# Kernel optimization log

Measured on AMD Instinct MI355X. Metric: run time of the kernel, lower is better.

Reference implementation:

```python
import jax, jax.numpy as jnp
import numpy as np

NUM_TABLES = 26
ROWS = 100000
EMB = 64
B = 4096
L = 32  # num_lookups per bag
BOT = [256, 512, 256, 64]
TOP = [EMB * (1 + NUM_TABLES), 512, 256, 1]


def _mlp_params(key, dims):
    params = []
    for i in range(len(dims) - 1):
        din, dout = dims[i], dims[i + 1]
        kw, kb, key = jax.random.split(key, 3)
        sw = np.sqrt(2.0 / (din + dout)).astype(np.float32)
        sb = np.sqrt(1.0 / dout).astype(np.float32)
        params.append((jax.random.normal(kw, (dout, din), jnp.float32) * sw,
                       jax.random.normal(kb, (dout,), jnp.float32) * sb))
    return params


def setup_inputs() -> dict:
    key = jax.random.key(0)
    k0, k1, k2, k3, k4 = jax.random.split(key, 5)
    inp = {}
    inp["x_dense"] = jax.random.normal(k0, (B, BOT[0]), jnp.float32)
    inp["x_indices"] = jax.random.randint(k1, (NUM_TABLES, B, L), 0, ROWS)
    bound = np.sqrt(1.0 / ROWS).astype(np.float32)
    inp["emb_tables"] = jax.random.uniform(k2, (NUM_TABLES, ROWS, EMB), jnp.float32, -bound, bound)
    for i, (w, b) in enumerate(_mlp_params(k3, BOT)):
        inp[f"bot_w{i}"] = w
        inp[f"bot_b{i}"] = b
    for i, (w, b) in enumerate(_mlp_params(k4, TOP)):
        inp[f"top_w{i}"] = w
        inp[f"top_b{i}"] = b
    return inp


def _forward(x_dense, x_indices, emb_tables, bot, top):
    # bottom MLP: Linear+ReLU per layer
    h = x_dense
    for w, b in bot:
        h = jax.nn.relu(h @ w.T + b)
    # multi-table EmbeddingBag(mode='sum'): gather rows then sum over bag dim
    # pooled: [T, B, E]
    pooled = jax.vmap(lambda tbl, idx: jnp.take(tbl, idx, axis=0).sum(axis=1))(emb_tables, x_indices)
    emb = jnp.transpose(pooled, (1, 0, 2)).reshape(x_dense.shape[0], -1)  # [B, T*E]
    z = jnp.concatenate([h, emb], axis=1)  # [B, E*(1+T)]
    # top MLP: ReLU on all but last, sigmoid on last
    n = len(top)
    for i, (w, b) in enumerate(top):
        z = z @ w.T + b
        z = jax.nn.sigmoid(z) if i == n - 1 else jax.nn.relu(z)
    return z


def reference(x_dense, x_indices, emb_tables,
              bot_w0, bot_b0, bot_w1, bot_b1, bot_w2, bot_b2,
              top_w0, top_b0, top_w1, top_b1, top_w2, top_b2):
    bot = [(bot_w0, bot_b0), (bot_w1, bot_b1), (bot_w2, bot_b2)]
    top = [(top_w0, top_b0), (top_w1, top_b1), (top_w2, top_b2)]
    return _forward(x_dense, x_indices, emb_tables, bot, top)
```

## Files before the change

### kernel.cpp

```cpp
#include <hip/hip_runtime.h>
#include <hip/hip_bf16.h>
#include <math.h>

typedef __attribute__((ext_vector_type(8))) short short8;
typedef __attribute__((ext_vector_type(4))) float f32x4;

#define NUM_TABLES 26
#define ROWS 100000
#define EMB 64
#define BATCH 4096
#define LOOKUPS 32
#define ZDIM 1728
#define CAST_BLOCKS 512
#define EMBED_BLOCKS (NUM_TABLES * BATCH / 4)

__device__ __forceinline__ unsigned short f2bf(float f) {
  unsigned int u = __float_as_uint(f);
  u += 0x7FFFu + ((u >> 16) & 1u);
  return (unsigned short)(u >> 16);
}
__device__ __forceinline__ float bf2f(unsigned short h) {
  return __uint_as_float(((unsigned int)h) << 16);
}

__device__ __forceinline__ void gload16(const void* g, void* l) {
  __builtin_amdgcn_global_load_lds(
      (const __attribute__((address_space(1))) void*)g,
      (__attribute__((address_space(3))) void*)l, 16, 0, 0);
}

struct CastArgs {
  const float* s[6];
  unsigned short* d[6];
  int n4[6];
  int total;
};

__global__ void embed_cast(CastArgs a, const int* __restrict__ idx,
                           const float* __restrict__ tables,
                           unsigned short* __restrict__ z) {
  if (blockIdx.x < CAST_BLOCKS) {
    for (int i = blockIdx.x * blockDim.x + threadIdx.x; i < a.total;
         i += CAST_BLOCKS * blockDim.x) {
      int r = i;
      #pragma unroll
      for (int sg = 0; sg < 6; ++sg) {
        if (r < a.n4[sg]) {
          float4 v = ((const float4*)a.s[sg])[r];
          ushort4 o;
          o.x = f2bf(v.x); o.y = f2bf(v.y); o.z = f2bf(v.z); o.w = f2bf(v.w);
          ((ushort4*)a.d[sg])[r] = o;
          break;
        }
        r -= a.n4[sg];
      }
    }
    return;
  }
  int g = (int)(((blockIdx.x - CAST_BLOCKS) << 2) + (threadIdx.x >> 6));
  int lane = threadIdx.x & 63;
  int t = g >> 12;
  int b = g & 4095;
  const int* ip = idx + ((size_t)t * BATCH + b) * LOOKUPS;
  int myidx = (lane < LOOKUPS) ? ip[lane] : 0;
  const float* tbl = tables + (size_t)t * ROWS * EMB;
  int grp = lane >> 4;
  int e4 = lane & 15;
  float4 acc = {0.f, 0.f, 0.f, 0.f};
  #pragma unroll
  for (int it = 0; it < 8; ++it) {
    int r = __shfl(myidx, it * 4 + grp, 64);
    float4 v = ((const float4*)(tbl + (size_t)r * EMB))[e4];
    acc.x += v.x; acc.y += v.y; acc.z += v.z; acc.w += v.w;
  }
  #pragma unroll
  for (int m = 16; m <= 32; m <<= 1) {
    acc.x += __shfl_xor(acc.x, m, 64);
    acc.y += __shfl_xor(acc.y, m, 64);
    acc.z += __shfl_xor(acc.z, m, 64);
    acc.w += __shfl_xor(acc.w, m, 64);
  }
  if (lane < 16) {
    ushort4 o;
    o.x = f2bf(acc.x); o.y = f2bf(acc.y); o.z = f2bf(acc.z); o.w = f2bf(acc.w);
    *(ushort4*)&z[(size_t)b * ZDIM + EMB + t * EMB + e4 * 4] = o;
  }
}

template<int ACT>
__global__ __launch_bounds__(256) void gemm64s(
    const unsigned short* __restrict__ A,
    const unsigned short* __restrict__ W,
    const float* __restrict__ bias,
    unsigned short* __restrict__ C,
    int M, int N, int K, int ldc) {
  __shared__ unsigned short lds[2][64][64];

  int t = threadIdx.x;
  int lane = t & 63;
  int wid = t >> 6;
  int wr = wid >> 1;
  int wc = wid & 1;

  int ntn = N >> 6;
  int tm = blockIdx.x / ntn;
  int tn = blockIdx.x - tm * ntn;

  int srow = lane >> 3;
  int schunk = (lane & 7) ^ (srow & 7);
  const unsigned short* Ap0 = A + (size_t)(tm * 64 + wid * 16 + srow) * K + schunk * 8;
  const unsigned short* Wp0 = W + (size_t)(tn * 64 + wid * 16 + srow) * K + schunk * 8;
  size_t rowK8 = (size_t)8 * K;

  f32x4 acc[2][2];
  #pragma unroll
  for (int m = 0; m < 2; ++m)
    #pragma unroll
    for (int n = 0; n < 2; ++n)
      acc[m][n] = (f32x4){0.f, 0.f, 0.f, 0.f};

  int ra = wr * 32 + (lane & 15);
  int rb = wc * 32 + (lane & 15);
  int cidx = lane >> 4;
  int sA = ra & 7, sB = rb & 7;

  for (int k0 = 0; k0 < K; k0 += 64) {
    #pragma unroll
    for (int j = 0; j < 2; ++j) {
      gload16(Ap0 + (size_t)k0 + j * rowK8, &lds[0][wid * 16 + j * 8][0]);
      gload16(Wp0 + (size_t)k0 + j * rowK8, &lds[1][wid * 16 + j * 8][0]);
    }
    __syncthreads();

    const char* bA = (const char*)&lds[0][0][0];
    const char* bB = (const char*)&lds[1][0][0];
    #pragma unroll
    for (int kc = 0; kc < 2; ++kc) {
      int c = kc * 4 + cidx;
      short8 a0 = *(const short8*)(bA + ra * 128 + ((c ^ sA) << 4));
      short8 a1 = *(const short8*)(bA + (ra + 16) * 128 + ((c ^ sA) << 4));
      short8 b0 = *(const short8*)(bB + rb * 128 + ((c ^ sB) << 4));
      short8 b1 = *(const short8*)(bB + (rb + 16) * 128 + ((c ^ sB) << 4));
      acc[0][0] = __builtin_amdgcn_mfma_f32_16x16x32_bf16(a0, b0, acc[0][0], 0, 0, 0);
      acc[0][1] = __builtin_amdgcn_mfma_f32_16x16x32_bf16(a0, b1, acc[0][1], 0, 0, 0);
      acc[1][0] = __builtin_amdgcn_mfma_f32_16x16x32_bf16(a1, b0, acc[1][0], 0, 0, 0);
      acc[1][1] = __builtin_amdgcn_mfma_f32_16x16x32_bf16(a1, b1, acc[1][1], 0, 0, 0);
    }
    __syncthreads();
  }

  #pragma unroll
  for (int m = 0; m < 2; ++m) {
    int drow = tm * 64 + wr * 32 + m * 16 + ((lane >> 4) << 2);
    #pragma unroll
    for (int n = 0; n < 2; ++n) {
      int dcol = tn * 64 + wc * 32 + n * 16 + (lane & 15);
      float bv = bias[dcol];
      #pragma unroll
      for (int r = 0; r < 4; ++r) {
        float v = acc[m][n][r] + bv;
        if (ACT == 1) v = v > 0.f ? v : 0.f;
        C[(size_t)(drow + r) * ldc + dcol] = f2bf(v);
      }
    }
  }
}

template<int ACT>
__global__ void gemm16(const unsigned short* __restrict__ A,
                       const unsigned short* __restrict__ W,
                       const float* __restrict__ bias,
                       unsigned short* __restrict__ C,
                       int M, int N, int K, int ldc) {
  int lane = threadIdx.x & 63;
  int gw = (int)((blockIdx.x * blockDim.x + threadIdx.x) >> 6);
  int ntn = N >> 4;
  int tm = gw / ntn;
  int tn = gw - tm * ntn;
  if (tm >= (M >> 4)) return;

  int arow = (tm << 4) + (lane & 15);
  int wrow = (tn << 4) + (lane & 15);
  int kb = (lane >> 4) << 3;

  const short8* Ap = (const short8*)(A + (size_t)arow * K + kb);
  const short8* Wp = (const short8*)(W + (size_t)wrow * K + kb);

  f32x4 acc = {0.f, 0.f, 0.f, 0.f};
  int steps = K >> 5;
  #pragma unroll 8
  for (int s = 0; s < steps; ++s) {
    short8 a = Ap[s * 4];
    short8 b = Wp[s * 4];
    acc = __builtin_amdgcn_mfma_f32_16x16x32_bf16(a, b, acc, 0, 0, 0);
  }

  int dcol = (tn << 4) + (lane & 15);
  int drow = (tm << 4) + ((lane >> 4) << 2);
  float bv = bias[dcol];
  #pragma unroll
  for (int r = 0; r < 4; ++r) {
    float v = acc[r] + bv;
    if (ACT == 1) v = v > 0.f ? v : 0.f;
    C[(size_t)(drow + r) * ldc + dcol] = f2bf(v);
  }
}

__global__ void final_layer(const unsigned short* __restrict__ z2,
                            const float* __restrict__ w,
                            const float* __restrict__ bias,
                            float* __restrict__ out) {
  int g = (int)((blockIdx.x * blockDim.x + threadIdx.x) >> 6);
  int lane = threadIdx.x & 63;
  const unsigned short* zp = z2 + (size_t)g * 256;
  float s = 0.f;
  #pragma unroll
  for (int k = 0; k < 256; k += 64)
    s += bf2f(zp[k + lane]) * w[k + lane];
  #pragma unroll
  for (int off = 32; off > 0; off >>= 1)
    s += __shfl_down(s, off, 64);
  if (lane == 0) out[g] = 1.f / (1.f + expf(-(s + bias[0])));
}

extern "C" void kernel_launch(void* const* d_in, const int* in_sizes, int n_in,
                              void* d_out, int out_size, void* d_ws, size_t ws_size,
                              hipStream_t stream) {
  const float* x_dense = (const float*)d_in[0];
  const int*   x_idx   = (const int*)d_in[1];
  const float* tables  = (const float*)d_in[2];
  const float* bw0 = (const float*)d_in[3];  const float* bb0 = (const float*)d_in[4];
  const float* bw1 = (const float*)d_in[5];  const float* bb1 = (const float*)d_in[6];
  const float* bw2 = (const float*)d_in[7];  const float* bb2 = (const float*)d_in[8];
  const float* tw0 = (const float*)d_in[9];  const float* tb0 = (const float*)d_in[10];
  const float* tw1 = (const float*)d_in[11]; const float* tb1 = (const float*)d_in[12];
  const float* tw2 = (const float*)d_in[13]; const float* tb2 = (const float*)d_in[14];
  float* out = (float*)d_out;

  char* ws = (char*)d_ws;
  size_t off = 0;
  auto alloc = [&](size_t bytes) { void* p = ws + off; off += (bytes + 255) & ~(size_t)255; return p; };
  unsigned short* xdb  = (unsigned short*)alloc((size_t)BATCH * 256 * 2);
  unsigned short* bw0b = (unsigned short*)alloc((size_t)512 * 256 * 2);
  unsigned short* bw1b = (unsigned short*)alloc((size_t)256 * 512 * 2);
  unsigned short* bw2b = (unsigned short*)alloc((size_t)64 * 256 * 2);
  unsigned short* tw0b = (unsigned short*)alloc((size_t)512 * ZDIM * 2);
  unsigned short* tw1b = (unsigned short*)alloc((size_t)256 * 512 * 2);
  unsigned short* h0   = (unsigned short*)alloc((size_t)BATCH * 512 * 2);
  unsigned short* h1   = (unsigned short*)alloc((size_t)BATCH * 256 * 2);
  unsigned short* z    = (unsigned short*)alloc((size_t)BATCH * ZDIM * 2);
  unsigned short* z1   = (unsigned short*)alloc((size_t)BATCH * 512 * 2);
  unsigned short* z2   = (unsigned short*)alloc((size_t)BATCH * 256 * 2);

  {
    CastArgs a;
    a.s[0] = x_dense; a.d[0] = xdb;  a.n4[0] = BATCH * 256 / 4;
    a.s[1] = bw0;     a.d[1] = bw0b; a.n4[1] = 512 * 256 / 4;
    a.s[2] = bw1;     a.d[2] = bw1b; a.n4[2] = 256 * 512 / 4;
    a.s[3] = bw2;     a.d[3] = bw2b; a.n4[3] = 64 * 256 / 4;
    a.s[4] = tw0;     a.d[4] = tw0b; a.n4[4] = 512 * ZDIM / 4;
    a.s[5] = tw1;     a.d[5] = tw1b; a.n4[5] = 256 * 512 / 4;
    a.total = a.n4[0] + a.n4[1] + a.n4[2] + a.n4[3] + a.n4[4] + a.n4[5];
    embed_cast<<<CAST_BLOCKS + EMBED_BLOCKS, 256, 0, stream>>>(a, x_idx, tables, z);
  }

  auto gemm = [&](const unsigned short* A, const unsigned short* W, const float* bias,
                  unsigned short* C, int M, int N, int K, int ldc, int relu) {
    if (N >= 128) {
      int blocks = (M >> 6) * (N >> 6);
      if (relu)
        gemm64s<1><<<blocks, 256, 0, stream>>>(A, W, bias, C, M, N, K, ldc);
      else
        gemm64s<0><<<blocks, 256, 0, stream>>>(A, W, bias, C, M, N, K, ldc);
    } else {
      int tiles = (M >> 4) * (N >> 4);
      if (relu)
        gemm16<1><<<tiles / 4, 256, 0, stream>>>(A, W, bias, C, M, N, K, ldc);
      else
        gemm16<0><<<tiles / 4, 256, 0, stream>>>(A, W, bias, C, M, N, K, ldc);
    }
  };

  gemm(xdb, bw0b, bb0, h0, BATCH, 512, 256, 512, 1);
  gemm(h0,  bw1b, bb1, h1, BATCH, 256, 512, 256, 1);
  gemm(h1,  bw2b, bb2, z,  BATCH, 64, 256, ZDIM, 1);

  gemm(z,  tw0b, tb0, z1, BATCH, 512, ZDIM, 512, 1);
  gemm(z1, tw1b, tb1, z2, BATCH, 256, 512, 256, 1);

  final_layer<<<BATCH / 4, 256, 0, stream>>>(z2, tw2, tb2, out);
}
```

Measured before the change: 182.2 us.

## Fuse bottom MLP into embedding kernel with per-block LDS-resident activations

Moves the three bottom-MLP layers into the same launch as the embedding-bag gather. Each of the new blocks handles 16 batch rows, keeps intermediate activations in swizzled LDS, and converts fp32 weights to bf16 on the fly instead of using a separate cast pass. This removes three GEMM launches, the cast of the bottom weights and input, and the global round trips for h0/h1, and lets the bottom MLP overlap with the memory-bound gather. The cost is that every block re-reads the full bottom weight matrices from global/L2 and converts them redundantly. The bottom-MLP blocks may also underuse MFMA because each handles only 16 rows.

Result: faster. 177.1 us (-2.8%).

```diff
diff --git a/kernel.cpp b/kernel.cpp
--- a/kernel.cpp
+++ b/kernel.cpp
@@ -11,7 +11,9 @@
 #define BATCH 4096
 #define LOOKUPS 32
 #define ZDIM 1728
-#define CAST_BLOCKS 512
+
+#define CAST_BLOCKS 128
+#define BOT_BLOCKS 256
 #define EMBED_BLOCKS (NUM_TABLES * BATCH / 4)
 
 __device__ __forceinline__ unsigned short f2bf(float f) {
@@ -29,41 +31,163 @@
       (__attribute__((address_space(3))) void*)l, 16, 0, 0);
 }
 
-struct CastArgs {
-  const float* s[6];
-  unsigned short* d[6];
-  int n4[6];
-  int total;
+__device__ __forceinline__ short8 wfrag_f32(const float* __restrict__ W, int K,
+                                            int colbase, int l, int kc) {
+  const float* p = W + (size_t)(colbase + (l & 15)) * K + kc * 32 + ((l >> 4) << 3);
+  float4 u = *(const float4*)p;
+  float4 v = *(const float4*)(p + 4);
+  short8 f;
+  f[0] = (short)f2bf(u.x); f[1] = (short)f2bf(u.y);
+  f[2] = (short)f2bf(u.z); f[3] = (short)f2bf(u.w);
+  f[4] = (short)f2bf(v.x); f[5] = (short)f2bf(v.y);
+  f[6] = (short)f2bf(v.z); f[7] = (short)f2bf(v.w);
+  return f;
+}
+
+struct MegaArgs {
+  const float* cast_s[2];
+  unsigned short* cast_d[2];
+  int cast_n4[2];
+  int cast_total;
+  const float* x_dense;
+  const float* bw0; const float* bb0;
+  const float* bw1; const float* bb1;
+  const float* bw2; const float* bb2;
+  const int* idx;
+  const float* tables;
+  unsigned short* z;
 };
 
-__global__ void embed_cast(CastArgs a, const int* __restrict__ idx,
-                           const float* __restrict__ tables,
-                           unsigned short* __restrict__ z) {
+__global__ void mega(MegaArgs a) {
+  __shared__ unsigned short xb[16][256];
+  __shared__ unsigned short h0[16][512];
+
   if (blockIdx.x < CAST_BLOCKS) {
-    for (int i = blockIdx.x * blockDim.x + threadIdx.x; i < a.total;
+    for (int i = blockIdx.x * blockDim.x + threadIdx.x; i < a.cast_total;
          i += CAST_BLOCKS * blockDim.x) {
       int r = i;
       #pragma unroll
-      for (int sg = 0; sg < 6; ++sg) {
-        if (r < a.n4[sg]) {
-          float4 v = ((const float4*)a.s[sg])[r];
+      for (int sg = 0; sg < 2; ++sg) {
+        if (r < a.cast_n4[sg]) {
+          float4 v = ((const float4*)a.cast_s[sg])[r];
           ushort4 o;
           o.x = f2bf(v.x); o.y = f2bf(v.y); o.z = f2bf(v.z); o.w = f2bf(v.w);
-          ((ushort4*)a.d[sg])[r] = o;
+          ((ushort4*)a.cast_d[sg])[r] = o;
           break;
         }
-        r -= a.n4[sg];
+        r -= a.cast_n4[sg];
       }
     }
     return;
   }
-  int g = (int)(((blockIdx.x - CAST_BLOCKS) << 2) + (threadIdx.x >> 6));
+
+  if (blockIdx.x < CAST_BLOCKS + BOT_BLOCKS) {
+    int b0 = (int)(blockIdx.x - CAST_BLOCKS) << 4;
+    int w = threadIdx.x >> 6;
+    int l = threadIdx.x & 63;
+
+    #pragma unroll
+    for (int i = 0; i < 4; ++i) {
+      int flat = i * 256 + threadIdx.x;
+      int row = flat >> 6;
+      int c4 = flat & 63;
+      float4 v = *(const float4*)(a.x_dense + (size_t)(b0 + row) * 256 + c4 * 4);
+      int chunk = c4 >> 1;
+      int scol = ((chunk ^ (row & 7)) << 3) | ((c4 & 1) << 2);
+      ushort4 o;
+      o.x = f2bf(v.x); o.y = f2bf(v.y); o.z = f2bf(v.z); o.w = f2bf(v.w);
+      *(ushort4*)&xb[row][scol] = o;
+    }
+    __syncthreads();
+
+    int arow = l & 15;
+    int sA = arow & 7;
+    const char* xbp = (const char*)&xb[0][0];
+    const char* h0p = (const char*)&h0[0][0];
+
+    f32x4 acc0[8];
+    #pragma unroll
+    for (int n = 0; n < 8; ++n) acc0[n] = (f32x4){0.f, 0.f, 0.f, 0.f};
+    for (int kc = 0; kc < 8; ++kc) {
+      int c = kc * 4 + (l >> 4);
+      short8 av = *(const short8*)(xbp + arow * 512 + ((c ^ sA) << 4));
+      #pragma unroll
+      for (int n = 0; n < 8; ++n) {
+        short8 bv = wfrag_f32(a.bw0, 256, w * 128 + n * 16, l, kc);
+        acc0[n] = __builtin_amdgcn_mfma_f32_16x16x32_bf16(av, bv, acc0[n], 0, 0, 0);
+      }
+    }
+    #pragma unroll
+    for (int n = 0; n < 8; ++n) {
+      int col = w * 128 + n * 16 + (l & 15);
+      float bv = a.bb0[col];
+      int chunk = col >> 3;
+      #pragma unroll
+      for (int r = 0; r < 4; ++r) {
+        int row = ((l >> 4) << 2) + r;
+        float val = acc0[n][r] + bv;
+        val = val > 0.f ? val : 0.f;
+        h0[row][((chunk ^ (row & 7)) << 3) | (col & 7)] = f2bf(val);
+      }
+    }
+    __syncthreads();
+
+    f32x4 acc1[4];
+    #pragma unroll
+    for (int n = 0; n < 4; ++n) acc1[n] = (f32x4){0.f, 0.f, 0.f, 0.f};
+    for (int kc = 0; kc < 16; ++kc) {
+      int c = kc * 4 + (l >> 4);
+      short8 av = *(const short8*)(h0p + arow * 1024 + ((c ^ sA) << 4));
+      #pragma unroll
+      for (int n = 0; n < 4; ++n) {
+        short8 bv = wfrag_f32(a.bw1, 512, w * 64 + n * 16, l, kc);
+        acc1[n] = __builtin_amdgcn_mfma_f32_16x16x32_bf16(av, bv, acc1[n], 0, 0, 0);
+      }
+    }
+    __syncthreads();
+    #pragma unroll
+    for (int n = 0; n < 4; ++n) {
+      int col = w * 64 + n * 16 + (l & 15);
+      float bv = a.bb1[col];
+      int chunk = col >> 3;
+      #pragma unroll
+      for (int r = 0; r < 4; ++r) {
+        int row = ((l >> 4) << 2) + r;
+        float val = acc1[n][r] + bv;
+        val = val > 0.f ? val : 0.f;
+        xb[row][((chunk ^ (row & 7)) << 3) | (col & 7)] = f2bf(val);
+      }
+    }
+    __syncthreads();
+
+    f32x4 acc2 = (f32x4){0.f, 0.f, 0.f, 0.f};
+    for (int kc = 0; kc < 8; ++kc) {
+      int c = kc * 4 + (l >> 4);
+      short8 av = *(const short8*)(xbp + arow * 512 + ((c ^ sA) << 4));
+      short8 bv = wfrag_f32(a.bw2, 256, w * 16, l, kc);
+      acc2 = __builtin_amdgcn_mfma_f32_16x16x32_bf16(av, bv, acc2, 0, 0, 0);
+    }
+    {
+      int col = w * 16 + (l & 15);
+      float bv = a.bb2[col];
+      #pragma unroll
+      for (int r = 0; r < 4; ++r) {
+        int row = ((l >> 4) << 2) + r;
+        float val = acc2[r] + bv;
+        val = val > 0.f ? val : 0.f;
+        a.z[(size_t)(b0 + row) * ZDIM + col] = f2bf(val);
+      }
+    }
+    return;
+  }
+
+  int g = (int)(((blockIdx.x - CAST_BLOCKS - BOT_BLOCKS) << 2) + (threadIdx.x >> 6));
   int lane = threadIdx.x & 63;
   int t = g >> 12;
   int b = g & 4095;
-  const int* ip = idx + ((size_t)t * BATCH + b) * LOOKUPS;
+  const int* ip = a.idx + ((size_t)t * BATCH + b) * LOOKUPS;
   int myidx = (lane < LOOKUPS) ? ip[lane] : 0;
-  const float* tbl = tables + (size_t)t * ROWS * EMB;
+  const float* tbl = a.tables + (size_t)t * ROWS * EMB;
   int grp = lane >> 4;
   int e4 = lane & 15;
   float4 acc = {0.f, 0.f, 0.f, 0.f};
@@ -83,7 +207,7 @@
   if (lane < 16) {
     ushort4 o;
     o.x = f2bf(acc.x); o.y = f2bf(acc.y); o.z = f2bf(acc.z); o.w = f2bf(acc.w);
-    *(ushort4*)&z[(size_t)b * ZDIM + EMB + t * EMB + e4 * 4] = o;
+    *(ushort4*)&a.z[(size_t)b * ZDIM + EMB + t * EMB + e4 * 4] = o;
   }
 }
 
@@ -163,46 +287,6 @@
         C[(size_t)(drow + r) * ldc + dcol] = f2bf(v);
       }
     }
-  }
-}
-
-template<int ACT>
-__global__ void gemm16(const unsigned short* __restrict__ A,
-                       const unsigned short* __restrict__ W,
-                       const float* __restrict__ bias,
-                       unsigned short* __restrict__ C,
-                       int M, int N, int K, int ldc) {
-  int lane = threadIdx.x & 63;
-  int gw = (int)((blockIdx.x * blockDim.x + threadIdx.x) >> 6);
-  int ntn = N >> 4;
-  int tm = gw / ntn;
-  int tn = gw - tm * ntn;
-  if (tm >= (M >> 4)) return;
-
-  int arow = (tm << 4) + (lane & 15);
-  int wrow = (tn << 4) + (lane & 15);
-  int kb = (lane >> 4) << 3;
-
-  const short8* Ap = (const short8*)(A + (size_t)arow * K + kb);
-  const short8* Wp = (const short8*)(W + (size_t)wrow * K + kb);
-
-  f32x4 acc = {0.f, 0.f, 0.f, 0.f};
-  int steps = K >> 5;
-  #pragma unroll 8
-  for (int s = 0; s < steps; ++s) {
-    short8 a = Ap[s * 4];
-    short8 b = Wp[s * 4];
-    acc = __builtin_amdgcn_mfma_f32_16x16x32_bf16(a, b, acc, 0, 0, 0);
-  }
-
-  int dcol = (tn << 4) + (lane & 15);
-  int drow = (tm << 4) + ((lane >> 4) << 2);
-  float bv = bias[dcol];
-  #pragma unroll
-  for (int r = 0; r < 4; ++r) {
-    float v = acc[r] + bv;
-    if (ACT == 1) v = v > 0.f ? v : 0.f;
-    C[(size_t)(drow + r) * ldc + dcol] = f2bf(v);
   }
 }
 
@@ -240,50 +324,35 @@
   char* ws = (char*)d_ws;
   size_t off = 0;
   auto alloc = [&](size_t bytes) { void* p = ws + off; off += (bytes + 255) & ~(size_t)255; return p; };
-  unsigned short* xdb  = (unsigned short*)alloc((size_t)BATCH * 256 * 2);
-  unsigned short* bw0b = (unsigned short*)alloc((size_t)512 * 256 * 2);
-  unsigned short* bw1b = (unsigned short*)alloc((size_t)256 * 512 * 2);
-  unsigned short* bw2b = (unsigned short*)alloc((size_t)64 * 256 * 2);
   unsigned short* tw0b = (unsigned short*)alloc((size_t)512 * ZDIM * 2);
   unsigned short* tw1b = (unsigned short*)alloc((size_t)256 * 512 * 2);
-  unsigned short* h0   = (unsigned short*)alloc((size_t)BATCH * 512 * 2);
-  unsigned short* h1   = (unsigned short*)alloc((size_t)BATCH * 256 * 2);
   unsigned short* z    = (unsigned short*)alloc((size_t)BATCH * ZDIM * 2);
   unsigned short* z1   = (unsigned short*)alloc((size_t)BATCH * 512 * 2);
   unsigned short* z2   = (unsigned short*)alloc((size_t)BATCH * 256 * 2);
 
   {
-    CastArgs a;
-    a.s[0] = x_dense; a.d[0] = xdb;  a.n4[0] = BATCH * 256 / 4;
-    a.s[1] = bw0;     a.d[1] = bw0b; a.n4[1] = 512 * 256 / 4;
-    a.s[2] = bw1;     a.d[2] = bw1b; a.n4[2] = 256 * 512 / 4;
-    a.s[3] = bw2;     a.d[3] = bw2b; a.n4[3] = 64 * 256 / 4;
-    a.s[4] = tw0;     a.d[4] = tw0b; a.n4[4] = 512 * ZDIM / 4;
-    a.s[5] = tw1;     a.d[5] = tw1b; a.n4[5] = 256 * 512 / 4;
-    a.total = a.n4[0] + a.n4[1] + a.n4[2] + a.n4[3] + a.n4[4] + a.n4[5];
-    embed_cast<<<CAST_BLOCKS + EMBED_BLOCKS, 256, 0, stream>>>(a, x_idx, tables, z);
+    MegaArgs a;
+    a.cast_s[0] = tw0; a.cast_d[0] = tw0b; a.cast_n4[0] = 512 * ZDIM / 4;
+    a.cast_s[1] = tw1; a.cast_d[1] = tw1b; a.cast_n4[1] = 256 * 512 / 4;
+    a.cast_total = a.cast_n4[0] + a.cast_n4[1];
+    a.x_dense = x_dense;
+    a.bw0 = bw0; a.bb0 = bb0;
+    a.bw1 = bw1; a.bb1 = bb1;
+    a.bw2 = bw2; a.bb2 = bb2;
+    a.idx = x_idx;
+    a.tables = tables;
+    a.z = z;
+    mega<<<CAST_BLOCKS + BOT_BLOCKS + EMBED_BLOCKS, 256, 0, stream>>>(a);
   }
 
   auto gemm = [&](const unsigned short* A, const unsigned short* W, const float* bias,
                   unsigned short* C, int M, int N, int K, int ldc, int relu) {
-    if (N >= 128) {
-      int blocks = (M >> 6) * (N >> 6);
-      if (relu)
-        gemm64s<1><<<blocks, 256, 0, stream>>>(A, W, bias, C, M, N, K, ldc);
-      else
-        gemm64s<0><<<blocks, 256, 0, stream>>>(A, W, bias, C, M, N, K, ldc);
-    } else {
-      int tiles = (M >> 4) * (N >> 4);
-      if (relu)
-        gemm16<1><<<tiles / 4, 256, 0, stream>>>(A, W, bias, C, M, N, K, ldc);
-      else
-        gemm16<0><<<tiles / 4, 256, 0, stream>>>(A, W, bias, C, M, N, K, ldc);
-    }
+    int blocks = (M >> 6) * (N >> 6);
+    if (relu)
+      gemm64s<1><<<blocks, 256, 0, stream>>>(A, W, bias, C, M, N, K, ldc);
+    else
+      gemm64s<0><<<blocks, 256, 0, stream>>>(A, W, bias, C, M, N, K, ldc);
   };
-
-  gemm(xdb, bw0b, bb0, h0, BATCH, 512, 256, 512, 1);
-  gemm(h0,  bw1b, bb1, h1, BATCH, 256, 512, 256, 1);
-  gemm(h1,  bw2b, bb2, z,  BATCH, 64, 256, ZDIM, 1);
 
   gemm(z,  tw0b, tb0, z1, BATCH, 512, ZDIM, 512, 1);
   gemm(z1, tw1b, tb1, z2, BATCH, 256, 512, 256, 1);
```
